# Kernel tuning notes

Hardware: AMD Instinct MI355X
Metric: run time of the kernel (lower is better)

Reference implementation:

```python
import jax, jax.numpy as jnp
import numpy as np

EMBED = 1024
HEADS = 16
HEAD_DIM = EMBED // HEADS
B, L = 4, 2048


def setup_inputs() -> dict:
    key = jax.random.key(0)
    ks = jax.random.split(key, 10)
    s = 1.0 / np.sqrt(EMBED)
    x = jax.random.normal(ks[0], (B, L, EMBED), dtype=jnp.float32)
    mask = jax.random.randint(ks[1], (B, 1, L, L), 0, 2, dtype=jnp.int32)
    Wq = jax.random.normal(ks[2], (EMBED, EMBED), dtype=jnp.float32) * s
    Wk = jax.random.normal(ks[3], (EMBED, EMBED), dtype=jnp.float32) * s
    Wv = jax.random.normal(ks[4], (EMBED, EMBED), dtype=jnp.float32) * s
    Wo = jax.random.normal(ks[5], (EMBED, EMBED), dtype=jnp.float32) * s
    bq = jnp.zeros((EMBED,), jnp.float32)
    bk = jnp.zeros((EMBED,), jnp.float32)
    bv = jnp.zeros((EMBED,), jnp.float32)
    bo = jnp.zeros((EMBED,), jnp.float32)
    return {"x": x, "mask": mask, "Wq": Wq, "bq": bq, "Wk": Wk, "bk": bk,
            "Wv": Wv, "bv": bv, "Wo": Wo, "bo": bo}


def reference(x, mask, Wq, bq, Wk, bk, Wv, bv, Wo, bo):
    n, l, _ = x.shape
    q = (x @ Wq + bq).reshape(n, l, HEADS, HEAD_DIM)
    k = (x @ Wk + bk).reshape(n, l, HEADS, HEAD_DIM)
    v = (x @ Wv + bv).reshape(n, l, HEADS, HEAD_DIM)
    # [n, h, q, k] scores
    energy = jnp.einsum('nqhd,nkhd->nhqk', q, k)
    energy = jnp.where(mask == 0, jnp.float32(-1e20), energy)
    attn = jax.nn.softmax(energy / jnp.sqrt(jnp.float32(HEAD_DIM)), axis=-1)
    out = jnp.einsum('nhqk,nkhd->nqhd', attn, v).reshape(n, l, EMBED)
    return out @ Wo + bo
```

## Files before the change

### kernel.cpp

```cpp
#include <hip/hip_runtime.h>
#include <hip/hip_bf16.h>

#define EMBED 1024
#define HEADS 16
#define HDIM 64
#define BATCH 4
#define SEQ 2048
#define ROWS (BATCH * SEQ)
#define LOG2E 1.4426950408889634f

typedef __attribute__((ext_vector_type(8))) short bf16x8;
typedef __attribute__((ext_vector_type(4))) float f32x4;

#define MFMA16(a, b, c) __builtin_amdgcn_mfma_f32_16x16x32_bf16(a, b, c, 0, 0, 0)

__device__ __forceinline__ unsigned short f2bf(float f) {
    union { float f; unsigned int u; } x; x.f = f;
    unsigned int r = x.u + 0x7fffu + ((x.u >> 16) & 1u);
    return (unsigned short)(r >> 16);
}

__device__ __forceinline__ ushort2 pk2(float a, float b) {
    union { __hip_bfloat162 h; ushort2 u; } c;
    c.h = __float22bfloat162_rn(make_float2(a, b));
    return c.u;
}

__device__ __forceinline__ void gl2lds(const unsigned short* g, unsigned short* l) {
    __builtin_amdgcn_global_load_lds(
        (const __attribute__((address_space(1))) unsigned int*)g,
        (__attribute__((address_space(3))) unsigned int*)l, 16, 0, 0);
}

__global__ __launch_bounds__(256) void cvt_x_kernel(
    const float* __restrict__ in, unsigned short* __restrict__ out)
{
    int i = (blockIdx.x * 256 + threadIdx.x) * 4;
    float4 v = *(const float4*)(in + i);
    ushort2 a = pk2(v.x, v.y), b = pk2(v.z, v.w);
    ushort4 o; o.x = a.x; o.y = a.y; o.z = b.x; o.w = b.y;
    *(ushort4*)(out + i) = o;
}

__global__ __launch_bounds__(256) void wtrans_kernel(
    const float* __restrict__ W0, const float* __restrict__ W1,
    const float* __restrict__ W2, const float* __restrict__ W3,
    unsigned short* __restrict__ Wt)
{
    __shared__ float t[32][33];
    const float* W = (blockIdx.z == 0) ? W0 : (blockIdx.z == 1) ? W1
                   : (blockIdx.z == 2) ? W2 : W3;
    unsigned short* o = Wt + (size_t)blockIdx.z * EMBED * EMBED;
    int tx = threadIdx.x & 31, ty = threadIdx.x >> 5;
    int bx = blockIdx.x * 32, by = blockIdx.y * 32;
#pragma unroll
    for (int r = 0; r < 32; r += 8)
        t[ty + r][tx] = W[(size_t)(by + ty + r) * EMBED + bx + tx];
    __syncthreads();
#pragma unroll
    for (int r = 0; r < 32; r += 8)
        o[(size_t)(bx + ty + r) * EMBED + by + tx] = f2bf(t[tx][ty + r]);
}

__global__ __launch_bounds__(256) void cvt_mask_kernel(
    const int* __restrict__ in, unsigned char* __restrict__ out)
{
    int i = (blockIdx.x * 256 + threadIdx.x) * 4;
    int4 v = *(const int4*)(in + i);
    uchar4 o;
    o.x = v.x != 0; o.y = v.y != 0; o.z = v.z != 0; o.w = v.w != 0;
    *(uchar4*)(out + i) = o;
}

__global__ __launch_bounds__(256) void vtrans_kernel(
    const unsigned short* __restrict__ Vb, unsigned short* __restrict__ Vt)
{
    __shared__ unsigned short t[64][72];
    int b = blockIdx.z, h = blockIdx.y, k0 = blockIdx.x * 64;
    int r = threadIdx.x >> 2, c = (threadIdx.x & 3) * 16;
    const unsigned short* src = Vb + (size_t)(b * SEQ + k0 + r) * EMBED + h * HDIM + c;
    *(uint4*)&t[r][c]     = *(const uint4*)(src);
    *(uint4*)&t[r][c + 8] = *(const uint4*)(src + 8);
    __syncthreads();
    unsigned short* dst = Vt + (size_t)((b * HEADS + h) * HDIM + r) * SEQ + k0 + c;
    union { unsigned short u[8]; uint4 v; } p0, p1;
#pragma unroll
    for (int i = 0; i < 8; i++) p0.u[i] = t[c + i][r];
#pragma unroll
    for (int i = 0; i < 8; i++) p1.u[i] = t[c + 8 + i][r];
    *(uint4*)dst       = p0.v;
    *(uint4*)(dst + 8) = p1.v;
}

__device__ __forceinline__ void gemm_bf16_body(
    const unsigned short* __restrict__ A, const unsigned short* __restrict__ Bt,
    const float* __restrict__ bias,
    float* __restrict__ outF, unsigned short* __restrict__ outB, float scale)
{
    __shared__ unsigned short As[128][32];
    __shared__ unsigned short Bs[128][32];
    const int tid = threadIdx.x;
    const int lane = tid & 63, wid = tid >> 6;
    const int ln = lane & 15, lg = lane >> 4;
    const int wy = wid >> 1, wx = wid & 1;
    const int m0 = blockIdx.y * 128, n0 = blockIdx.x * 128;
    const int srow = tid >> 2;
    const int scol = (((tid & 3) ^ ((tid >> 2) & 3) ^ ((tid >> 4) & 3)) << 3);
    const unsigned short* Ap = A + (size_t)(m0 + srow) * EMBED + scol;
    const unsigned short* Bp = Bt + (size_t)(n0 + srow) * EMBED + scol;
    unsigned short* lA = &As[srow & ~15][0];
    unsigned short* lB = &Bs[srow & ~15][0];
    const int swg = ((lg ^ (ln & 3) ^ (ln >> 2)) << 3);

    f32x4 acc[4][4];
#pragma unroll
    for (int i = 0; i < 4; i++)
#pragma unroll
        for (int j = 0; j < 4; j++) acc[i][j] = (f32x4){0.f, 0.f, 0.f, 0.f};

    for (int k0 = 0; k0 < EMBED; k0 += 32) {
        __syncthreads();
        gl2lds(Ap + k0, lA);
        gl2lds(Ap + (size_t)64 * EMBED + k0, lA + 64 * 32);
        gl2lds(Bp + k0, lB);
        gl2lds(Bp + (size_t)64 * EMBED + k0, lB + 64 * 32);
        __syncthreads();
        bf16x8 af[4], bfr[4];
#pragma unroll
        for (int mi = 0; mi < 4; mi++)
            af[mi] = *(const bf16x8*)&As[wy * 64 + mi * 16 + ln][swg];
#pragma unroll
        for (int nj = 0; nj < 4; nj++)
            bfr[nj] = *(const bf16x8*)&Bs[wx * 64 + nj * 16 + ln][swg];
#pragma unroll
        for (int mi = 0; mi < 4; mi++)
#pragma unroll
            for (int nj = 0; nj < 4; nj++)
                acc[mi][nj] = MFMA16(af[mi], bfr[nj], acc[mi][nj]);
    }

#pragma unroll
    for (int mi = 0; mi < 4; mi++) {
#pragma unroll
        for (int nj = 0; nj < 4; nj++) {
            int row = m0 + wy * 64 + mi * 16 + lg * 4;
            int col = n0 + wx * 64 + nj * 16 + ln;
            float bv = bias[col];
#pragma unroll
            for (int r = 0; r < 4; r++) {
                float v = (acc[mi][nj][r] + bv) * scale;
                if (outF) outF[(size_t)(row + r) * EMBED + col] = v;
                else      outB[(size_t)(row + r) * EMBED + col] = f2bf(v);
            }
        }
    }
}

__global__ __launch_bounds__(256) void qkv_gemm_kernel(
    const unsigned short* __restrict__ Xb, const unsigned short* __restrict__ Wt,
    const float* __restrict__ bq, const float* __restrict__ bk,
    const float* __restrict__ bv,
    unsigned short* __restrict__ Qb, unsigned short* __restrict__ Kb,
    unsigned short* __restrict__ Vb)
{
    int z = blockIdx.z;
    const unsigned short* Bt = Wt + (size_t)z * EMBED * EMBED;
    const float* bias = (z == 0) ? bq : (z == 1) ? bk : bv;
    unsigned short* out = (z == 0) ? Qb : (z == 1) ? Kb : Vb;
    float scale = (z == 0) ? 0.125f * LOG2E : 1.0f;
    gemm_bf16_body(Xb, Bt, bias, nullptr, out, scale);
}

__global__ __launch_bounds__(256) void out_gemm_kernel(
    const unsigned short* __restrict__ Ob, const unsigned short* __restrict__ Wto,
    const float* __restrict__ bo, float* __restrict__ out)
{
    gemm_bf16_body(Ob, Wto, bo, out, nullptr, 1.0f);
}

__global__ __launch_bounds__(256) void attn_mfma_kernel(
    const unsigned short* __restrict__ Qb, const unsigned short* __restrict__ Kb,
    const unsigned short* __restrict__ Vt, const unsigned char* __restrict__ mask8,
    unsigned short* __restrict__ Ob)
{
    __shared__ unsigned short Ks[64][64];
    __shared__ unsigned short Vs[64][64];
    __shared__ unsigned short Ps[4][32][64];
    const int tid = threadIdx.x;
    const int lane = tid & 63, wid = tid >> 6;
    const int ln = lane & 15, lg = lane >> 4;
    const int b = blockIdx.z, h = blockIdx.y;
    const int q0 = blockIdx.x * 128 + wid * 32;

    bf16x8 qf[2][2];
#pragma unroll
    for (int mi = 0; mi < 2; mi++)
#pragma unroll
        for (int ks = 0; ks < 2; ks++)
            qf[mi][ks] = *(const bf16x8*)(Qb +
                (size_t)(b * SEQ + q0 + mi * 16 + ln) * EMBED + h * HDIM + ks * 32 + lg * 8);

    bf16x8 ones;
#pragma unroll
    for (int i = 0; i < 8; i++) ones[i] = (short)0x3F80;

    f32x4 o[2][4];
#pragma unroll
    for (int mi = 0; mi < 2; mi++)
#pragma unroll
        for (int dj = 0; dj < 4; dj++) o[mi][dj] = (f32x4){0.f, 0.f, 0.f, 0.f};
    f32x4 lacc[2] = {(f32x4){0.f, 0.f, 0.f, 0.f}, (f32x4){0.f, 0.f, 0.f, 0.f}};

    const int srow = tid >> 3;
    const int scolKV = (((tid & 7) ^ ((tid >> 3) & 7)) << 3);
    const unsigned short* Kp = Kb + (size_t)(b * SEQ + srow) * EMBED + h * HDIM + scolKV;
    const unsigned short* Vp = Vt + (size_t)((b * HEADS + h) * HDIM + srow) * SEQ + scolKV;
    unsigned short* lK = &Ks[srow & ~7][0];
    unsigned short* lV = &Vs[srow & ~7][0];

    const unsigned char* mq0 = mask8 + (size_t)b * SEQ * SEQ + (size_t)(q0 + ln) * SEQ;
    const unsigned char* mq1 = mq0 + (size_t)16 * SEQ;

    const int swk = ((lg ^ (ln & 7)) << 3);

    int pwr[4], prd[2];
#pragma unroll
    for (int nj = 0; nj < 4; nj++)
        pwr[nj] = (((2 * nj + (lg >> 1)) ^ (ln & 7)) << 3) + ((lg & 1) << 2);
#pragma unroll
    for (int ks = 0; ks < 2; ks++)
        prd[ks] = ((4 * ks + lg) ^ (ln & 7)) << 3;
    unsigned short* ps0 = &Ps[wid][ln][0];
    unsigned short* ps1 = &Ps[wid][16 + ln][0];

    for (int kt = 0; kt < SEQ; kt += 64) {
        uchar4 mv[2][4];
#pragma unroll
        for (int mi = 0; mi < 2; mi++) {
            const unsigned char* mq = (mi ? mq1 : mq0) + kt;
#pragma unroll
            for (int nj = 0; nj < 4; nj++)
                mv[mi][nj] = *(const uchar4*)(mq + nj * 16 + lg * 4);
        }

        __syncthreads();
        gl2lds(Kp + (size_t)kt * EMBED, lK);
        gl2lds(Kp + (size_t)(kt + 32) * EMBED, lK + 32 * 64);
        gl2lds(Vp + kt, lV);
        gl2lds(Vp + (size_t)32 * SEQ + kt, lV + 32 * 64);
        __syncthreads();

        f32x4 S[2][4];
#pragma unroll
        for (int nj = 0; nj < 4; nj++) {
            bf16x8 k0 = *(const bf16x8*)&Ks[nj * 16 + ln][swk];
            bf16x8 k1 = *(const bf16x8*)&Ks[nj * 16 + ln][swk ^ 32];
#pragma unroll
            for (int mi = 0; mi < 2; mi++) {
                f32x4 t = (f32x4){0.f, 0.f, 0.f, 0.f};
                t = MFMA16(k0, qf[mi][0], t);
                t = MFMA16(k1, qf[mi][1], t);
                S[mi][nj] = t;
            }
        }

#pragma unroll
        for (int mi = 0; mi < 2; mi++) {
            unsigned short* psb = mi ? ps1 : ps0;
#pragma unroll
            for (int nj = 0; nj < 4; nj++) {
                uchar4 m = mv[mi][nj];
                float p0 = m.x ? __builtin_amdgcn_exp2f(S[mi][nj][0]) : 0.f;
                float p1 = m.y ? __builtin_amdgcn_exp2f(S[mi][nj][1]) : 0.f;
                float p2 = m.z ? __builtin_amdgcn_exp2f(S[mi][nj][2]) : 0.f;
                float p3 = m.w ? __builtin_amdgcn_exp2f(S[mi][nj][3]) : 0.f;
                ushort2 w0 = pk2(p0, p1), w1 = pk2(p2, p3);
                ushort4 pw; pw.x = w0.x; pw.y = w0.y; pw.z = w1.x; pw.w = w1.y;
                *(ushort4*)(psb + pwr[nj]) = pw;
            }
        }

#pragma unroll
        for (int ks = 0; ks < 2; ks++) {
            bf16x8 p0 = *(const bf16x8*)(ps0 + prd[ks]);
            bf16x8 p1 = *(const bf16x8*)(ps1 + prd[ks]);
            lacc[0] = MFMA16(p0, ones, lacc[0]);
            lacc[1] = MFMA16(p1, ones, lacc[1]);
#pragma unroll
            for (int dj = 0; dj < 4; dj++) {
                bf16x8 vf = *(const bf16x8*)&Vs[dj * 16 + ln][swk ^ (ks << 5)];
                o[0][dj] = MFMA16(p0, vf, o[0][dj]);
                o[1][dj] = MFMA16(p1, vf, o[1][dj]);
            }
        }
    }

#pragma unroll
    for (int mi = 0; mi < 2; mi++) {
        float l0 = 1.0f / lacc[mi][0];
        float l1 = 1.0f / lacc[mi][1];
        float l2 = 1.0f / lacc[mi][2];
        float l3 = 1.0f / lacc[mi][3];
#pragma unroll
        for (int dj = 0; dj < 4; dj++) {
            unsigned short* op = Ob + (size_t)(b * SEQ + q0 + mi * 16 + lg * 4) * EMBED
                                    + h * HDIM + dj * 16 + ln;
            ushort2 w0 = pk2(o[mi][dj][0] * l0, o[mi][dj][1] * l1);
            ushort2 w1 = pk2(o[mi][dj][2] * l2, o[mi][dj][3] * l3);
            op[0]         = w0.x;
            op[EMBED]     = w0.y;
            op[2 * EMBED] = w1.x;
            op[3 * EMBED] = w1.y;
        }
    }
}

extern "C" void kernel_launch(void* const* d_in, const int* in_sizes, int n_in,
                              void* d_out, int out_size, void* d_ws, size_t ws_size,
                              hipStream_t stream)
{
    const float* x  = (const float*)d_in[0];
    const int* mask = (const int*)d_in[1];
    const float* Wq = (const float*)d_in[2];
    const float* bq = (const float*)d_in[3];
    const float* Wk = (const float*)d_in[4];
    const float* bk = (const float*)d_in[5];
    const float* Wv = (const float*)d_in[6];
    const float* bv = (const float*)d_in[7];
    const float* Wo = (const float*)d_in[8];
    const float* bo = (const float*)d_in[9];
    float* outp = (float*)d_out;

    char* ws = (char*)d_ws;
    unsigned short* Wt = (unsigned short*)(ws);
    unsigned char*  m8 = (unsigned char*)(ws + ((size_t)8 << 20));
    unsigned short* Xb = (unsigned short*)(ws + ((size_t)24 << 20));
    unsigned short* Vt = Xb;
    unsigned short* Qb = (unsigned short*)(ws + ((size_t)40 << 20));
    unsigned short* Kb = (unsigned short*)(ws + ((size_t)56 << 20));
    unsigned short* Vb = (unsigned short*)(ws + ((size_t)72 << 20));
    unsigned short* Ob = Vb;

    cvt_x_kernel<<<ROWS * EMBED / 1024, 256, 0, stream>>>(x, Xb);
    wtrans_kernel<<<dim3(32, 32, 4), 256, 0, stream>>>(Wq, Wk, Wv, Wo, Wt);
    cvt_mask_kernel<<<(size_t)BATCH * SEQ * SEQ / 1024, 256, 0, stream>>>(mask, m8);
    qkv_gemm_kernel<<<dim3(EMBED / 128, ROWS / 128, 3), 256, 0, stream>>>(
        Xb, Wt, bq, bk, bv, Qb, Kb, Vb);
    vtrans_kernel<<<dim3(SEQ / 64, HEADS, BATCH), 256, 0, stream>>>(Vb, Vt);
    attn_mfma_kernel<<<dim3(SEQ / 128, HEADS, BATCH), 256, 0, stream>>>(
        Qb, Kb, Vt, m8, Ob);
    out_gemm_kernel<<<dim3(EMBED / 128, ROWS / 128), 256, 0, stream>>>(
        Ob, Wt + (size_t)3 * EMBED * EMBED, bo, outp);
}
```

Baseline: 417.7 us.

## Double-buffer K/V tiles in attention, fuse V transpose into QKV GEMM epilogue

```diff
diff --git a/kernel.cpp b/kernel.cpp
--- a/kernel.cpp
+++ b/kernel.cpp
@@ -20,10 +20,14 @@
     return (unsigned short)(r >> 16);
 }
 
-__device__ __forceinline__ ushort2 pk2(float a, float b) {
-    union { __hip_bfloat162 h; ushort2 u; } c;
-    c.h = __float22bfloat162_rn(make_float2(a, b));
-    return c.u;
+__device__ __forceinline__ unsigned int pkbf(float a, float b) {
+#if __has_builtin(__builtin_amdgcn_cvt_pk_bf16_f32)
+    auto v = __builtin_amdgcn_cvt_pk_bf16_f32(a, b);
+    unsigned int u; __builtin_memcpy(&u, &v, 4); return u;
+#else
+    union { __hip_bfloat162 h; unsigned int u; } c;
+    c.h = __float22bfloat162_rn(make_float2(a, b)); return c.u;
+#endif
 }
 
 __device__ __forceinline__ void gl2lds(const unsigned short* g, unsigned short* l) {
@@ -37,9 +41,8 @@
 {
     int i = (blockIdx.x * 256 + threadIdx.x) * 4;
     float4 v = *(const float4*)(in + i);
-    ushort2 a = pk2(v.x, v.y), b = pk2(v.z, v.w);
-    ushort4 o; o.x = a.x; o.y = a.y; o.z = b.x; o.w = b.y;
-    *(ushort4*)(out + i) = o;
+    uint2 o; o.x = pkbf(v.x, v.y); o.y = pkbf(v.z, v.w);
+    *(uint2*)(out + i) = o;
 }
 
 __global__ __launch_bounds__(256) void wtrans_kernel(
@@ -68,34 +71,16 @@
     int i = (blockIdx.x * 256 + threadIdx.x) * 4;
     int4 v = *(const int4*)(in + i);
     uchar4 o;
-    o.x = v.x != 0; o.y = v.y != 0; o.z = v.z != 0; o.w = v.w != 0;
+    o.x = v.x ? 0xFF : 0; o.y = v.y ? 0xFF : 0;
+    o.z = v.z ? 0xFF : 0; o.w = v.w ? 0xFF : 0;
     *(uchar4*)(out + i) = o;
-}
-
-__global__ __launch_bounds__(256) void vtrans_kernel(
-    const unsigned short* __restrict__ Vb, unsigned short* __restrict__ Vt)
-{
-    __shared__ unsigned short t[64][72];
-    int b = blockIdx.z, h = blockIdx.y, k0 = blockIdx.x * 64;
-    int r = threadIdx.x >> 2, c = (threadIdx.x & 3) * 16;
-    const unsigned short* src = Vb + (size_t)(b * SEQ + k0 + r) * EMBED + h * HDIM + c;
-    *(uint4*)&t[r][c]     = *(const uint4*)(src);
-    *(uint4*)&t[r][c + 8] = *(const uint4*)(src + 8);
-    __syncthreads();
-    unsigned short* dst = Vt + (size_t)((b * HEADS + h) * HDIM + r) * SEQ + k0 + c;
-    union { unsigned short u[8]; uint4 v; } p0, p1;
-#pragma unroll
-    for (int i = 0; i < 8; i++) p0.u[i] = t[c + i][r];
-#pragma unroll
-    for (int i = 0; i < 8; i++) p1.u[i] = t[c + 8 + i][r];
-    *(uint4*)dst       = p0.v;
-    *(uint4*)(dst + 8) = p1.v;
 }
 
 __device__ __forceinline__ void gemm_bf16_body(
     const unsigned short* __restrict__ A, const unsigned short* __restrict__ Bt,
     const float* __restrict__ bias,
-    float* __restrict__ outF, unsigned short* __restrict__ outB, float scale)
+    float* __restrict__ outF, unsigned short* __restrict__ outB, float scale,
+    int vmode)
 {
     __shared__ unsigned short As[128][32];
     __shared__ unsigned short Bs[128][32];
@@ -146,11 +131,22 @@
             int row = m0 + wy * 64 + mi * 16 + lg * 4;
             int col = n0 + wx * 64 + nj * 16 + ln;
             float bv = bias[col];
-#pragma unroll
-            for (int r = 0; r < 4; r++) {
-                float v = (acc[mi][nj][r] + bv) * scale;
-                if (outF) outF[(size_t)(row + r) * EMBED + col] = v;
-                else      outB[(size_t)(row + r) * EMBED + col] = f2bf(v);
+            if (vmode) {
+                int bb = row >> 11, s = row & (SEQ - 1);
+                int hh = col >> 6, dd = col & 63;
+                unsigned short* dst = outB +
+                    ((size_t)((bb * HEADS + hh) * HDIM + dd)) * SEQ + s;
+                uint2 pw;
+                pw.x = pkbf(acc[mi][nj][0] + bv, acc[mi][nj][1] + bv);
+                pw.y = pkbf(acc[mi][nj][2] + bv, acc[mi][nj][3] + bv);
+                *(uint2*)dst = pw;
+            } else {
+#pragma unroll
+                for (int r = 0; r < 4; r++) {
+                    float v = (acc[mi][nj][r] + bv) * scale;
+                    if (outF) outF[(size_t)(row + r) * EMBED + col] = v;
+                    else      outB[(size_t)(row + r) * EMBED + col] = f2bf(v);
+                }
             }
         }
     }
@@ -161,21 +157,21 @@
     const float* __restrict__ bq, const float* __restrict__ bk,
     const float* __restrict__ bv,
     unsigned short* __restrict__ Qb, unsigned short* __restrict__ Kb,
-    unsigned short* __restrict__ Vb)
+    unsigned short* __restrict__ Vt)
 {
     int z = blockIdx.z;
     const unsigned short* Bt = Wt + (size_t)z * EMBED * EMBED;
     const float* bias = (z == 0) ? bq : (z == 1) ? bk : bv;
-    unsigned short* out = (z == 0) ? Qb : (z == 1) ? Kb : Vb;
+    unsigned short* out = (z == 0) ? Qb : (z == 1) ? Kb : Vt;
     float scale = (z == 0) ? 0.125f * LOG2E : 1.0f;
-    gemm_bf16_body(Xb, Bt, bias, nullptr, out, scale);
+    gemm_bf16_body(Xb, Bt, bias, nullptr, out, scale, z == 2);
 }
 
 __global__ __launch_bounds__(256) void out_gemm_kernel(
     const unsigned short* __restrict__ Ob, const unsigned short* __restrict__ Wto,
     const float* __restrict__ bo, float* __restrict__ out)
 {
-    gemm_bf16_body(Ob, Wto, bo, out, nullptr, 1.0f);
+    gemm_bf16_body(Ob, Wto, bo, out, nullptr, 1.0f, 0);
 }
 
 __global__ __launch_bounds__(256) void attn_mfma_kernel(
@@ -183,8 +179,8 @@
     const unsigned short* __restrict__ Vt, const unsigned char* __restrict__ mask8,
     unsigned short* __restrict__ Ob)
 {
-    __shared__ unsigned short Ks[64][64];
-    __shared__ unsigned short Vs[64][64];
+    __shared__ unsigned short Ks[2][64][64];
+    __shared__ unsigned short Vs[2][64][64];
     __shared__ unsigned short Ps[4][32][64];
     const int tid = threadIdx.x;
     const int lane = tid & 63, wid = tid >> 6;
@@ -215,8 +211,8 @@
     const int scolKV = (((tid & 7) ^ ((tid >> 3) & 7)) << 3);
     const unsigned short* Kp = Kb + (size_t)(b * SEQ + srow) * EMBED + h * HDIM + scolKV;
     const unsigned short* Vp = Vt + (size_t)((b * HEADS + h) * HDIM + srow) * SEQ + scolKV;
-    unsigned short* lK = &Ks[srow & ~7][0];
-    unsigned short* lV = &Vs[srow & ~7][0];
+    unsigned short* lK[2] = {&Ks[0][srow & ~7][0], &Ks[1][srow & ~7][0]};
+    unsigned short* lV[2] = {&Vs[0][srow & ~7][0], &Vs[1][srow & ~7][0]};
 
     const unsigned char* mq0 = mask8 + (size_t)b * SEQ * SEQ + (size_t)(q0 + ln) * SEQ;
     const unsigned char* mq1 = mq0 + (size_t)16 * SEQ;
@@ -233,34 +229,45 @@
     unsigned short* ps0 = &Ps[wid][ln][0];
     unsigned short* ps1 = &Ps[wid][16 + ln][0];
 
-    for (int kt = 0; kt < SEQ; kt += 64) {
-        uchar4 mv[2][4];
+    gl2lds(Kp, lK[0]);
+    gl2lds(Kp + (size_t)32 * EMBED, lK[0] + 32 * 64);
+    gl2lds(Vp, lV[0]);
+    gl2lds(Vp + (size_t)32 * SEQ, lV[0] + 32 * 64);
+
+    const int NT = SEQ / 64;
+    for (int t = 0; t < NT; t++) {
+        const int cur = t & 1;
+        const int kt = t * 64;
+        __syncthreads();
+
+        unsigned int mw[2][4];
 #pragma unroll
         for (int mi = 0; mi < 2; mi++) {
             const unsigned char* mq = (mi ? mq1 : mq0) + kt;
 #pragma unroll
             for (int nj = 0; nj < 4; nj++)
-                mv[mi][nj] = *(const uchar4*)(mq + nj * 16 + lg * 4);
-        }
-
-        __syncthreads();
-        gl2lds(Kp + (size_t)kt * EMBED, lK);
-        gl2lds(Kp + (size_t)(kt + 32) * EMBED, lK + 32 * 64);
-        gl2lds(Vp + kt, lV);
-        gl2lds(Vp + (size_t)32 * SEQ + kt, lV + 32 * 64);
-        __syncthreads();
+                mw[mi][nj] = *(const unsigned int*)(mq + nj * 16 + lg * 4);
+        }
+
+        if (t + 1 < NT) {
+            const int nk = kt + 64;
+            gl2lds(Kp + (size_t)nk * EMBED, lK[cur ^ 1]);
+            gl2lds(Kp + (size_t)(nk + 32) * EMBED, lK[cur ^ 1] + 32 * 64);
+            gl2lds(Vp + nk, lV[cur ^ 1]);
+            gl2lds(Vp + (size_t)(32 * SEQ) + nk, lV[cur ^ 1] + 32 * 64);
+        }
 
         f32x4 S[2][4];
 #pragma unroll
         for (int nj = 0; nj < 4; nj++) {
-            bf16x8 k0 = *(const bf16x8*)&Ks[nj * 16 + ln][swk];
-            bf16x8 k1 = *(const bf16x8*)&Ks[nj * 16 + ln][swk ^ 32];
+            bf16x8 k0 = *(const bf16x8*)&Ks[cur][nj * 16 + ln][swk];
+            bf16x8 k1 = *(const bf16x8*)&Ks[cur][nj * 16 + ln][swk ^ 32];
 #pragma unroll
             for (int mi = 0; mi < 2; mi++) {
-                f32x4 t = (f32x4){0.f, 0.f, 0.f, 0.f};
-                t = MFMA16(k0, qf[mi][0], t);
-                t = MFMA16(k1, qf[mi][1], t);
-                S[mi][nj] = t;
+                f32x4 t2 = (f32x4){0.f, 0.f, 0.f, 0.f};
+                t2 = MFMA16(k0, qf[mi][0], t2);
+                t2 = MFMA16(k1, qf[mi][1], t2);
+                S[mi][nj] = t2;
             }
         }
 
@@ -269,14 +276,17 @@
             unsigned short* psb = mi ? ps1 : ps0;
 #pragma unroll
             for (int nj = 0; nj < 4; nj++) {
-                uchar4 m = mv[mi][nj];
-                float p0 = m.x ? __builtin_amdgcn_exp2f(S[mi][nj][0]) : 0.f;
-                float p1 = m.y ? __builtin_amdgcn_exp2f(S[mi][nj][1]) : 0.f;
-                float p2 = m.z ? __builtin_amdgcn_exp2f(S[mi][nj][2]) : 0.f;
-                float p3 = m.w ? __builtin_amdgcn_exp2f(S[mi][nj][3]) : 0.f;
-                ushort2 w0 = pk2(p0, p1), w1 = pk2(p2, p3);
-                ushort4 pw; pw.x = w0.x; pw.y = w0.y; pw.z = w1.x; pw.w = w1.y;
-                *(ushort4*)(psb + pwr[nj]) = pw;
+                float p0 = __builtin_amdgcn_exp2f(S[mi][nj][0]);
+                float p1 = __builtin_amdgcn_exp2f(S[mi][nj][1]);
+                float p2 = __builtin_amdgcn_exp2f(S[mi][nj][2]);
+                float p3 = __builtin_amdgcn_exp2f(S[mi][nj][3]);
+                unsigned int m = mw[mi][nj];
+                unsigned int d0 = __builtin_amdgcn_perm(0u, m, 0x01010000u);
+                unsigned int d1 = __builtin_amdgcn_perm(0u, m, 0x03030202u);
+                uint2 pw;
+                pw.x = pkbf(p0, p1) & d0;
+                pw.y = pkbf(p2, p3) & d1;
+                *(uint2*)(psb + pwr[nj]) = pw;
             }
         }
 
@@ -288,7 +298,7 @@
             lacc[1] = MFMA16(p1, ones, lacc[1]);
 #pragma unroll
             for (int dj = 0; dj < 4; dj++) {
-                bf16x8 vf = *(const bf16x8*)&Vs[dj * 16 + ln][swk ^ (ks << 5)];
+                bf16x8 vf = *(const bf16x8*)&Vs[cur][dj * 16 + ln][swk ^ (ks << 5)];
                 o[0][dj] = MFMA16(p0, vf, o[0][dj]);
                 o[1][dj] = MFMA16(p1, vf, o[1][dj]);
             }
@@ -305,12 +315,10 @@
         for (int dj = 0; dj < 4; dj++) {
             unsigned short* op = Ob + (size_t)(b * SEQ + q0 + mi * 16 + lg * 4) * EMBED
                                     + h * HDIM + dj * 16 + ln;
-            ushort2 w0 = pk2(o[mi][dj][0] * l0, o[mi][dj][1] * l1);
-            ushort2 w1 = pk2(o[mi][dj][2] * l2, o[mi][dj][3] * l3);
-            op[0]         = w0.x;
-            op[EMBED]     = w0.y;
-            op[2 * EMBED] = w1.x;
-            op[3 * EMBED] = w1.y;
+            op[0]         = f2bf(o[mi][dj][0] * l0);
+            op[EMBED]     = f2bf(o[mi][dj][1] * l1);
+            op[2 * EMBED] = f2bf(o[mi][dj][2] * l2);
+            op[3 * EMBED] = f2bf(o[mi][dj][3] * l3);
         }
     }
 }
@@ -335,18 +343,16 @@
     unsigned short* Wt = (unsigned short*)(ws);
     unsigned char*  m8 = (unsigned char*)(ws + ((size_t)8 << 20));
     unsigned short* Xb = (unsigned short*)(ws + ((size_t)24 << 20));
-    unsigned short* Vt = Xb;
+    unsigned short* Ob = Xb;
     unsigned short* Qb = (unsigned short*)(ws + ((size_t)40 << 20));
     unsigned short* Kb = (unsigned short*)(ws + ((size_t)56 << 20));
-    unsigned short* Vb = (unsigned short*)(ws + ((size_t)72 << 20));
-    unsigned short* Ob = Vb;
+    unsigned short* Vt = (unsigned short*)(ws + ((size_t)72 << 20));
 
     cvt_x_kernel<<<ROWS * EMBED / 1024, 256, 0, stream>>>(x, Xb);
     wtrans_kernel<<<dim3(32, 32, 4), 256, 0, stream>>>(Wq, Wk, Wv, Wo, Wt);
     cvt_mask_kernel<<<(size_t)BATCH * SEQ * SEQ / 1024, 256, 0, stream>>>(mask, m8);
     qkv_gemm_kernel<<<dim3(EMBED / 128, ROWS / 128, 3), 256, 0, stream>>>(
-        Xb, Wt, bq, bk, bv, Qb, Kb, Vb);
-    vtrans_kernel<<<dim3(SEQ / 64, HEADS, BATCH), 256, 0, stream>>>(Vb, Vt);
+        Xb, Wt, bq, bk, bv, Qb, Kb, Vt);
     attn_mfma_kernel<<<dim3(SEQ / 128, HEADS, BATCH), 256, 0, stream>>>(
         Qb, Kb, Vt, m8, Ob);
     out_gemm_kernel<<<dim3(EMBED / 128, ROWS / 128), 256, 0, stream>>>(
```

Result: slower. 427.8 us (+2.4%).
